# Performance work log

Measured on AMD Instinct MI355X. Metric: run time of the kernel, lower is better.

The kernel has to match this reference:

```python
import jax, jax.numpy as jnp
import numpy as np


def _mlp(x, w1, b1, w2, b2):
    # generic 2-layer MLP (stand-in for ConfiguredModule's combine_mlp / embedding_mlp)
    return jax.nn.gelu(x @ w1 + b1) @ w2 + b2


def setup_inputs() -> dict:
    key = jax.random.key(0)
    ks = jax.random.split(key, 8)
    B, N, A = 8, 128, 64          # molecules, atoms, nfeature
    Rr, Ra = 32, 16               # radial / angular geometry shifts
    P = N * (N - 1) // 2          # 8128 atom pairs
    d_pair, H, nembed = 32, 512, 256

    def rnd(k, shp, scale=1.0):
        return jax.random.normal(k, shp, dtype=jnp.float32) * scale

    return {
        "gr": rnd(ks[0], (B, N, Rr, N), 0.1),
        "ga": rnd(ks[1], (B, N, Ra, P), 0.1),
        "afv": rnd(ks[2], (B, N, A)),
        # combine_mlp: 2A -> 2A -> d_pair
        "cw1": rnd(ks[3], (2 * A, 2 * A), 1.0 / np.sqrt(2 * A)),
        "cb1": jnp.zeros((2 * A,), jnp.float32),
        "cw2": rnd(ks[4], (2 * A, d_pair), 1.0 / np.sqrt(2 * A)),
        "cb2": jnp.zeros((d_pair,), jnp.float32),
        # embedding_mlp: Rr*A + Ra*d_pair -> H -> nembed
        "ew1": rnd(ks[5], (Rr * A + Ra * d_pair, H), 1.0 / np.sqrt(Rr * A + Ra * d_pair)),
        "eb1": jnp.zeros((H,), jnp.float32),
        "ew2": rnd(ks[6], (H, nembed), 1.0 / np.sqrt(H)),
        "eb2": jnp.zeros((nembed,), jnp.float32),
    }


def reference(gr, ga, afv, cw1, cb1, cw2, cb2, ew1, eb1, ew2, eb2):
    B, N, A = afv.shape
    # _combine_afv_1: pairwise outer sum/product, upper-triangular (i<j) pairs.
    # Instead of materializing [B, 2A, N, N] and masking, gather pairs directly
    # (row-major i<j order matches torch's triu boolean-mask indexing).
    ii, jj = jnp.triu_indices(N, k=1)           # [P]
    ai = afv[:, ii, :]                           # [B, P, A]
    aj = afv[:, jj, :]                           # [B, P, A]
    afv_pair = jnp.concatenate([ai + aj, ai * aj], axis=-1)  # [B, P, 2A]
    afv_pair = _mlp(afv_pair, cw1, cb1, cw2, cb2)            # [B, P, d_pair]

    # grv = matmul(gr, afv[:, None]) : [B, N, Rr, N] @ [B, 1, N, A] -> [B, N, Rr, A]
    grv = jnp.einsum('bnrm,bma->bnra', gr, afv).reshape(B, N, -1)
    # gav = matmul(ga, afv_pair[:, None]) : [B, N, Ra, P] @ [B, 1, P, d] -> [B, N, Ra, d]
    gav = jnp.einsum('bnap,bpd->bnad', ga, afv_pair).reshape(B, N, -1)

    aef = _mlp(jnp.concatenate([grv, gav], axis=-1), ew1, eb1, ew2, eb2)  # [B, N, nembed]
    return aef, afv
```

## Files before the change

### kernel.cpp

```cpp
#include <hip/hip_runtime.h>
#include <math.h>

#define BB 8
#define NN 128
#define AA 64
#define RR 32
#define RA 16
#define PP 8128
#define DP 32
#define HH 512
#define EE 256
#define XDIM 2560

static constexpr size_t WS_PAIRT = 0;
static constexpr size_t WS_XB    = WS_PAIRT + (size_t)BB*DP*PP/2;
static constexpr size_t WS_EW1B  = WS_XB + (size_t)BB*NN*XDIM/2;
static constexpr size_t WS_AFVT  = WS_EW1B + (size_t)HH*XDIM/2;
static constexpr size_t WS_CW1T  = WS_AFVT + (size_t)BB*AA*NN/2;
static constexpr size_t WS_CW2T  = WS_CW1T + (size_t)128*128/2;
static constexpr size_t WS_EW2B  = WS_CW2T + (size_t)DP*128/2;
static constexpr size_t WS_HB    = WS_EW2B + (size_t)EE*HH/2;

typedef __attribute__((ext_vector_type(8))) short bf16x8;
typedef __attribute__((ext_vector_type(4))) float f32x4;

__device__ __forceinline__ float gelu_f(float x) {
    float u = 0.7978845608028654f * (x + 0.044715f * x * x * x);
    float au = fabsf(u);
    float e = __expf(-2.0f * au);
    float th = (1.0f - e) / (1.0f + e);
    th = copysignf(th, u);
    return 0.5f * x * (1.0f + th);
}

__device__ __forceinline__ unsigned short f2bf(float x) {
    union { float f; unsigned u; } v; v.f = x;
    unsigned r = v.u + 0x7fffu + ((v.u >> 16) & 1u);
    return (unsigned short)(r >> 16);
}

__device__ __forceinline__ bf16x8 pack_bf16x8(float4 a, float4 b) {
    bf16x8 r;
    r[0] = (short)f2bf(a.x); r[1] = (short)f2bf(a.y);
    r[2] = (short)f2bf(a.z); r[3] = (short)f2bf(a.w);
    r[4] = (short)f2bf(b.x); r[5] = (short)f2bf(b.y);
    r[6] = (short)f2bf(b.z); r[7] = (short)f2bf(b.w);
    return r;
}

__global__ __launch_bounds__(256) void prep_k(
    const float* __restrict__ afv, const float* __restrict__ cw1,
    const float* __restrict__ cw2, unsigned short* __restrict__ afvT,
    unsigned short* __restrict__ cw1T, unsigned short* __restrict__ cw2T,
    float* __restrict__ out2)
{
    const int bid = blockIdx.x, t = threadIdx.x;
    if (bid < 64) {
        int idx = bid * 256 + t;
        int b = idx >> 11;
        int rem = idx & 2047;
        int a = rem >> 5;
        int m0 = (rem & 31) * 4;
        ushort4 o;
        o.x = f2bf(afv[((size_t)b * NN + m0 + 0) * AA + a]);
        o.y = f2bf(afv[((size_t)b * NN + m0 + 1) * AA + a]);
        o.z = f2bf(afv[((size_t)b * NN + m0 + 2) * AA + a]);
        o.w = f2bf(afv[((size_t)b * NN + m0 + 3) * AA + a]);
        *(ushort4*)(afvT + ((size_t)b * AA + a) * NN + m0) = o;
        float4 v = *(const float4*)(afv + (size_t)idx * 4);
        *(float4*)(out2 + (size_t)idx * 4) = v;
    } else if (bid < 80) {
        int idx = (bid - 64) * 256 + t;
        int n = idx >> 5;
        int k0 = (idx & 31) * 4;
        ushort4 o;
        o.x = f2bf(cw1[(size_t)(k0 + 0) * 128 + n]);
        o.y = f2bf(cw1[(size_t)(k0 + 1) * 128 + n]);
        o.z = f2bf(cw1[(size_t)(k0 + 2) * 128 + n]);
        o.w = f2bf(cw1[(size_t)(k0 + 3) * 128 + n]);
        *(ushort4*)(cw1T + (size_t)n * 128 + k0) = o;
    } else {
        int idx = (bid - 80) * 256 + t;
        int d = idx >> 5;
        int k0 = (idx & 31) * 4;
        ushort4 o;
        o.x = f2bf(cw2[(size_t)(k0 + 0) * DP + d]);
        o.y = f2bf(cw2[(size_t)(k0 + 1) * DP + d]);
        o.z = f2bf(cw2[(size_t)(k0 + 2) * DP + d]);
        o.w = f2bf(cw2[(size_t)(k0 + 3) * DP + d]);
        *(ushort4*)(cw2T + (size_t)d * 128 + k0) = o;
    }
}

#define NB_GRV 256
#define NB_PAIR 1016

__global__ __launch_bounds__(256) void stage1_k(
    const float* __restrict__ afv, const unsigned short* __restrict__ cw1T,
    const float* __restrict__ cb1, const unsigned short* __restrict__ cw2T,
    const float* __restrict__ cb2, unsigned short* __restrict__ pairT,
    const float* __restrict__ gr, unsigned short* __restrict__ Xb,
    const unsigned short* __restrict__ afvT)
{
    __shared__ unsigned short sm[16384];
    __shared__ int iis[64], jjs[64];
    const int bid = blockIdx.x;
    const int t = threadIdx.x;
    const int w = t >> 6, lane = t & 63;
    const int lm = lane & 15, lg = lane >> 4;

    if (bid < NB_GRV) {
        const int b = bid >> 5;
        const int rbase = (bid & 31) * 128;
        const float* gab = gr + ((size_t)b * 4096 + rbase) * NN;
        unsigned short* As = sm;
        const int srow = t >> 1, half = t & 1;
        const float* arow = gab + (size_t)srow * NN + half * 64;
        #pragma unroll
        for (int q = 0; q < 8; ++q) {
            float4 x0 = *(const float4*)(arow + q * 8);
            float4 x1 = *(const float4*)(arow + q * 8 + 4);
            bf16x8 v = pack_bf16x8(x0, x1);
            int g = half * 8 + q;
            *(bf16x8*)(As + srow * 128 + ((g ^ (srow & 7)) * 8)) = v;
        }
        __syncthreads();
        const int wm = w * 32;
        f32x4 acc[2][4];
        #pragma unroll
        for (int i = 0; i < 2; ++i)
            #pragma unroll
            for (int j = 0; j < 4; ++j) acc[i][j] = 0.f;
        const unsigned short* Bb = afvT + (size_t)b * AA * NN;
        #pragma unroll
        for (int ks = 0; ks < 4; ++ks) {
            int g = ks * 4 + lg;
            int r0 = wm + lm, r1 = wm + 16 + lm;
            bf16x8 a0 = *(const bf16x8*)(As + r0 * 128 + ((g ^ (r0 & 7)) * 8));
            bf16x8 a1 = *(const bf16x8*)(As + r1 * 128 + ((g ^ (r1 & 7)) * 8));
            #pragma unroll
            for (int ni = 0; ni < 4; ++ni) {
                bf16x8 bv = *(const bf16x8*)(Bb + (size_t)(ni * 16 + lm) * NN + ks * 32 + lg * 8);
                acc[0][ni] = __builtin_amdgcn_mfma_f32_16x16x32_bf16(a0, bv, acc[0][ni], 0, 0, 0);
                acc[1][ni] = __builtin_amdgcn_mfma_f32_16x16x32_bf16(a1, bv, acc[1][ni], 0, 0, 0);
            }
        }
        __syncthreads();
        unsigned short* T = sm;
        #pragma unroll
        for (int mi = 0; mi < 2; ++mi)
            #pragma unroll
            for (int ni = 0; ni < 4; ++ni)
                #pragma unroll
                for (int r = 0; r < 4; ++r)
                    T[(wm + mi * 16 + lg * 4 + r) * 64 + ni * 16 + lm] =
                        f2bf(acc[mi][ni][r]);
        __syncthreads();
        #pragma unroll
        for (int q = 0; q < 4; ++q) {
            int idx = t + q * 256;
            int rr2 = idx >> 3, slot = idx & 7;
            bf16x8 v = *(const bf16x8*)(T + rr2 * 64 + slot * 8);
            int grow = rbase + rr2;
            *(bf16x8*)(Xb + ((size_t)(b * NN) + (grow >> 5)) * XDIM +
                       (grow & 31) * 64 + slot * 8) = v;
        }
        return;
    }

    const int bid2 = bid - NB_GRV;
    const int b = bid2 / 127;
    const int pbase = (bid2 % 127) * 64;
    unsigned short* X = sm;
    unsigned short* Hs = sm + 8192;

    if (t < 64) {
        int p = pbase + t;
        int i = 0;
        while (i < 126) {
            int nx = i + 1;
            int off = nx * 127 - (nx * (nx - 1)) / 2;
            if (off <= p) i = nx; else break;
        }
        int off = i * 127 - (i * (i - 1)) / 2;
        iis[t] = i;
        jjs[t] = i + 1 + (p - off);
    }
    __syncthreads();
    {
        int pp = t & 63, seg = t >> 6;
        const float* ar = afv + (size_t)(b * NN + iis[pp]) * AA + seg * 16;
        const float* br = afv + (size_t)(b * NN + jjs[pp]) * AA + seg * 16;
        float4 xa = *(const float4*)(ar),     xb2 = *(const float4*)(ar + 4);
        float4 xc = *(const float4*)(ar + 8), xd = *(const float4*)(ar + 12);
        float4 ya = *(const float4*)(br),     yb = *(const float4*)(br + 4);
        float4 yc = *(const float4*)(br + 8), yd = *(const float4*)(br + 12);
        float4 s0 = make_float4(xa.x + ya.x, xa.y + ya.y, xa.z + ya.z, xa.w + ya.w);
        float4 s1 = make_float4(xb2.x + yb.x, xb2.y + yb.y, xb2.z + yb.z, xb2.w + yb.w);
        float4 s2 = make_float4(xc.x + yc.x, xc.y + yc.y, xc.z + yc.z, xc.w + yc.w);
        float4 s3 = make_float4(xd.x + yd.x, xd.y + yd.y, xd.z + yd.z, xd.w + yd.w);
        float4 p0 = make_float4(xa.x * ya.x, xa.y * ya.y, xa.z * ya.z, xa.w * ya.w);
        float4 p1 = make_float4(xb2.x * yb.x, xb2.y * yb.y, xb2.z * yb.z, xb2.w * yb.w);
        float4 p2 = make_float4(xc.x * yc.x, xc.y * yc.y, xc.z * yc.z, xc.w * yc.w);
        float4 p3 = make_float4(xd.x * yd.x, xd.y * yd.y, xd.z * yd.z, xd.w * yd.w);
        int gs = seg * 2, gp = 8 + seg * 2, sw = pp & 7;
        *(bf16x8*)(X + pp * 128 + (((gs + 0) ^ sw) * 8)) = pack_bf16x8(s0, s1);
        *(bf16x8*)(X + pp * 128 + (((gs + 1) ^ sw) * 8)) = pack_bf16x8(s2, s3);
        *(bf16x8*)(X + pp * 128 + (((gp + 0) ^ sw) * 8)) = pack_bf16x8(p0, p1);
        *(bf16x8*)(X + pp * 128 + (((gp + 1) ^ sw) * 8)) = pack_bf16x8(p2, p3);
    }
    __syncthreads();
    const int wn = w * 32;
    f32x4 acc1[4][2];
    #pragma unroll
    for (int i = 0; i < 4; ++i)
        #pragma unroll
        for (int j = 0; j < 2; ++j) acc1[i][j] = 0.f;
    #pragma unroll
    for (int ks = 0; ks < 4; ++ks) {
        int g = ks * 4 + lg;
        bf16x8 a[4];
        #pragma unroll
        for (int mi = 0; mi < 4; ++mi) {
            int row = mi * 16 + lm;
            a[mi] = *(const bf16x8*)(X + row * 128 + ((g ^ (row & 7)) * 8));
        }
        #pragma unroll
        for (int ni = 0; ni < 2; ++ni) {
            bf16x8 bv = *(const bf16x8*)(cw1T + (size_t)(wn + ni * 16 + lm) * 128 +
                                         ks * 32 + lg * 8);
            #pragma unroll
            for (int mi = 0; mi < 4; ++mi)
                acc1[mi][ni] = __builtin_amdgcn_mfma_f32_16x16x32_bf16(
                    a[mi], bv, acc1[mi][ni], 0, 0, 0);
        }
    }
    #pragma unroll
    for (int ni = 0; ni < 2; ++ni) {
        int n = wn + ni * 16 + lm;
        float bb = cb1[n];
        int gn = n >> 3, ne = n & 7;
        #pragma unroll
        for (int mi = 0; mi < 4; ++mi)
            #pragma unroll
            for (int r = 0; r < 4; ++r) {
                int row = mi * 16 + lg * 4 + r;
                Hs[row * 128 + ((gn ^ (row & 7)) * 8 + ne)] =
                    f2bf(gelu_f(acc1[mi][ni][r] + bb));
            }
    }
    __syncthreads();
    f32x4 acc2[2];
    acc2[0] = 0.f; acc2[1] = 0.f;
    #pragma unroll
    for (int ks = 0; ks < 4; ++ks) {
        int row = w * 16 + lm;
        int g = ks * 4 + lg;
        bf16x8 a2 = *(const bf16x8*)(Hs + row * 128 + ((g ^ (row & 7)) * 8));
        #pragma unroll
        for (int ni = 0; ni < 2; ++ni) {
            bf16x8 bv = *(const bf16x8*)(cw2T + (size_t)(ni * 16 + lm) * 128 +
                                         ks * 32 + lg * 8);
            acc2[ni] = __builtin_amdgcn_mfma_f32_16x16x32_bf16(a2, bv, acc2[ni], 0, 0, 0);
        }
    }
    {
        unsigned short* T = sm;
        #pragma unroll
        for (int ni = 0; ni < 2; ++ni) {
            int d = ni * 16 + lm;
            float bb = cb2[d];
            #pragma unroll
            for (int r = 0; r < 4; ++r) {
                int p = w * 16 + lg * 4 + r;
                T[d * 64 + p] = f2bf(acc2[ni][r] + bb);
            }
        }
        __syncthreads();
        int d = t >> 3, slot = t & 7;
        bf16x8 v = *(const bf16x8*)(T + d * 64 + slot * 8);
        *(bf16x8*)(pairT + ((size_t)b * DP + d) * PP + pbase + slot * 8) = v;
    }
}

__global__ __launch_bounds__(256) void gav_k(
    const float* __restrict__ ga, const unsigned short* __restrict__ pairT,
    unsigned short* __restrict__ Xb,
    const float* __restrict__ ew1, unsigned short* __restrict__ ew1bT,
    const float* __restrict__ ew2, unsigned short* __restrict__ ew2bT)
{
    __shared__ unsigned short As[32 * 128];
    __shared__ unsigned short Bs[32 * 128];
    const int bid = blockIdx.x;
    const int t = threadIdx.x;

    if (bid >= 512 + 1280) {
        int q = (bid - (512 + 1280)) * 256 + t;
        int n = q & 255;
        int k0 = (q >> 8) * 4;
        ushort4 o;
        o.x = f2bf(ew2[(size_t)(k0 + 0) * EE + n]);
        o.y = f2bf(ew2[(size_t)(k0 + 1) * EE + n]);
        o.z = f2bf(ew2[(size_t)(k0 + 2) * EE + n]);
        o.w = f2bf(ew2[(size_t)(k0 + 3) * EE + n]);
        *(ushort4*)(ew2bT + (size_t)n * HH + k0) = o;
        return;
    }
    if (bid >= 512) {
        int q = (bid - 512) * 256 + t;
        int n = q & 511;
        int k0 = (q >> 9) * 4;
        ushort4 o;
        o.x = f2bf(ew1[(size_t)(k0 + 0) * HH + n]);
        o.y = f2bf(ew1[(size_t)(k0 + 1) * HH + n]);
        o.z = f2bf(ew1[(size_t)(k0 + 2) * HH + n]);
        o.w = f2bf(ew1[(size_t)(k0 + 3) * HH + n]);
        *(ushort4*)(ew1bT + (size_t)n * XDIM + k0) = o;
        return;
    }

    const int rt = bid & 63, b = bid >> 6;
    const int rbase = rt * 32;
    const int srow = t >> 3, slot = t & 7;
    const int w = t >> 6, lane = t & 63;
    const int lm = lane & 15, lg = lane >> 4;
    const int wr = (w & 1) * 16, wc = (w >> 1) * 16;

    f32x4 acc = 0.f;

    const float* gab = ga + (size_t)(b * 2048 + rbase) * PP;
    const unsigned short* pbT = pairT + (size_t)b * DP * PP;

    float4 ra[4];
    bf16x8 rb0, rb1;
    {
        int k0 = slot * 8;
        ra[0] = *(const float4*)(gab + (size_t)srow * PP + k0);
        ra[1] = *(const float4*)(gab + (size_t)srow * PP + k0 + 4);
        ra[2] = *(const float4*)(gab + (size_t)srow * PP + k0 + 64);
        ra[3] = *(const float4*)(gab + (size_t)srow * PP + k0 + 68);
        rb0 = *(const bf16x8*)(pbT + (size_t)srow * PP + k0);
        rb1 = *(const bf16x8*)(pbT + (size_t)srow * PP + k0 + 64);
    }

    for (int it = 0; it < 64; ++it) {
        __syncthreads();
        const int sw = srow & 7;
        const int g0 = (slot ^ sw) * 8;
        const int g1 = ((slot ^ sw) + 8) * 8;
        *(bf16x8*)(As + srow * 128 + g0) = pack_bf16x8(ra[0], ra[1]);
        *(bf16x8*)(As + srow * 128 + g1) = pack_bf16x8(ra[2], ra[3]);
        *(bf16x8*)(Bs + srow * 128 + g0) = rb0;
        *(bf16x8*)(Bs + srow * 128 + g1) = rb1;
        __syncthreads();
        if (it + 1 < 64) {
            int kn = (it + 1) * 128 + slot * 8;
            int k1 = kn + 64; if (k1 > PP - 8) k1 = PP - 8;
            ra[0] = *(const float4*)(gab + (size_t)srow * PP + kn);
            ra[1] = *(const float4*)(gab + (size_t)srow * PP + kn + 4);
            ra[2] = *(const float4*)(gab + (size_t)srow * PP + k1);
            ra[3] = *(const float4*)(gab + (size_t)srow * PP + k1 + 4);
            rb0 = *(const bf16x8*)(pbT + (size_t)srow * PP + kn);
            rb1 = *(const bf16x8*)(pbT + (size_t)srow * PP + k1);
        }
        if (it < 63) {
            #pragma unroll
            for (int ks = 0; ks < 4; ++ks) {
                int gg = ks * 4 + lg;
                int rowa = wr + lm;
                int rowb = wc + lm;
                bf16x8 a  = *(const bf16x8*)(As + rowa * 128 + ((gg ^ (rowa & 7)) * 8));
                bf16x8 bv = *(const bf16x8*)(Bs + rowb * 128 + ((gg ^ (rowb & 7)) * 8));
                acc = __builtin_amdgcn_mfma_f32_16x16x32_bf16(a, bv, acc, 0, 0, 0);
            }
        } else {
            #pragma unroll
            for (int ks = 0; ks < 2; ++ks) {
                int gg = ks * 4 + lg;
                int rowa = wr + lm;
                int rowb = wc + lm;
                bf16x8 a  = *(const bf16x8*)(As + rowa * 128 + ((gg ^ (rowa & 7)) * 8));
                bf16x8 bv = *(const bf16x8*)(Bs + rowb * 128 + ((gg ^ (rowb & 7)) * 8));
                acc = __builtin_amdgcn_mfma_f32_16x16x32_bf16(a, bv, acc, 0, 0, 0);
            }
        }
    }
    #pragma unroll
    for (int r = 0; r < 4; ++r) {
        int grow = rbase + wr + lg * 4 + r;
        int n = grow >> 4, a2 = grow & 15;
        int d = wc + lm;
        Xb[(size_t)(b * NN + n) * XDIM + 2048 + a2 * DP + d] = f2bf(acc[r]);
    }
}

__global__ __launch_bounds__(256) void mlp1_k(
    const unsigned short* __restrict__ Xb,
    const unsigned short* __restrict__ Wt,
    const float* __restrict__ eb1, unsigned short* __restrict__ Hb)
{
    __shared__ unsigned short As[32 * 64];
    __shared__ unsigned short Bs[64 * 64];
    const int bid = blockIdx.x;
    const int ct = bid & 7, rt = bid >> 3;
    const int rbase = rt * 32, nbase = ct * 64;
    const int t = threadIdx.x;
    const int w = t >> 6, lane = t & 63;
    const int lm = lane & 15, lg = lane >> 4;
    const int srow = t >> 3, sg = t & 7;

    f32x4 acc[2];
    acc[0] = 0.f; acc[1] = 0.f;

    const unsigned short* Arow  = Xb + (size_t)(rbase + srow) * XDIM;
    const unsigned short* Brow0 = Wt + (size_t)(nbase + srow) * XDIM;
    const unsigned short* Brow1 = Wt + (size_t)(nbase + srow + 32) * XDIM;

    bf16x8 rA, rB0, rB1;
    rA  = *(const bf16x8*)(Arow + sg * 8);
    rB0 = *(const bf16x8*)(Brow0 + sg * 8);
    rB1 = *(const bf16x8*)(Brow1 + sg * 8);

    for (int it = 0; it < 40; ++it) {
        __syncthreads();
        const int sw = srow & 7;
        *(bf16x8*)(As + srow * 64 + ((sg ^ sw) * 8)) = rA;
        *(bf16x8*)(Bs + srow * 64 + ((sg ^ sw) * 8)) = rB0;
        *(bf16x8*)(Bs + (srow + 32) * 64 + ((sg ^ sw) * 8)) = rB1;
        __syncthreads();
        if (it + 1 < 40) {
            int kn = (it + 1) * 64;
            rA  = *(const bf16x8*)(Arow + kn + sg * 8);
            rB0 = *(const bf16x8*)(Brow0 + kn + sg * 8);
            rB1 = *(const bf16x8*)(Brow1 + kn + sg * 8);
        }
        #pragma unroll
        for (int ks = 0; ks < 2; ++ks) {
            int g = ks * 4 + lg;
            int r0 = lm, r1 = 16 + lm, rb_ = w * 16 + lm;
            bf16x8 a0 = *(const bf16x8*)(As + r0 * 64 + ((g ^ (r0 & 7)) * 8));
            bf16x8 a1 = *(const bf16x8*)(As + r1 * 64 + ((g ^ (r1 & 7)) * 8));
            bf16x8 bv = *(const bf16x8*)(Bs + rb_ * 64 + ((g ^ (rb_ & 7)) * 8));
            acc[0] = __builtin_amdgcn_mfma_f32_16x16x32_bf16(a0, bv, acc[0], 0, 0, 0);
            acc[1] = __builtin_amdgcn_mfma_f32_16x16x32_bf16(a1, bv, acc[1], 0, 0, 0);
        }
    }
    const int col = nbase + w * 16 + lm;
    const float bb = eb1[col];
    #pragma unroll
    for (int mi = 0; mi < 2; ++mi)
        #pragma unroll
        for (int r = 0; r < 4; ++r) {
            int row = rbase + mi * 16 + lg * 4 + r;
            Hb[(size_t)row * HH + col] = f2bf(gelu_f(acc[mi][r] + bb));
        }
}

__global__ __launch_bounds__(256) void mlp2_k(
    const unsigned short* __restrict__ Hb,
    const unsigned short* __restrict__ Wt,
    const float* __restrict__ eb2, float* __restrict__ out)
{
    __shared__ unsigned short As[32 * 64];
    __shared__ unsigned short Bs[64 * 64];
    const int bid = blockIdx.x;
    const int ct = bid & 3, rt = bid >> 2;
    const int rbase = rt * 32, nbase = ct * 64;
    const int t = threadIdx.x;
    const int w = t >> 6, lane = t & 63;
    const int lm = lane & 15, lg = lane >> 4;
    const int srow = t >> 3, sg = t & 7;

    f32x4 acc[2];
    acc[0] = 0.f; acc[1] = 0.f;

    const unsigned short* Arow  = Hb + (size_t)(rbase + srow) * HH;
    const unsigned short* Brow0 = Wt + (size_t)(nbase + srow) * HH;
    const unsigned short* Brow1 = Wt + (size_t)(nbase + srow + 32) * HH;

    bf16x8 rA, rB0, rB1;
    rA  = *(const bf16x8*)(Arow + sg * 8);
    rB0 = *(const bf16x8*)(Brow0 + sg * 8);
    rB1 = *(const bf16x8*)(Brow1 + sg * 8);

    for (int it = 0; it < 8; ++it) {
        __syncthreads();
        const int sw = srow & 7;
        *(bf16x8*)(As + srow * 64 + ((sg ^ sw) * 8)) = rA;
        *(bf16x8*)(Bs + srow * 64 + ((sg ^ sw) * 8)) = rB0;
        *(bf16x8*)(Bs + (srow + 32) * 64 + ((sg ^ sw) * 8)) = rB1;
        __syncthreads();
        if (it + 1 < 8) {
            int kn = (it + 1) * 64;
            rA  = *(const bf16x8*)(Arow + kn + sg * 8);
            rB0 = *(const bf16x8*)(Brow0 + kn + sg * 8);
            rB1 = *(const bf16x8*)(Brow1 + kn + sg * 8);
        }
        #pragma unroll
        for (int ks = 0; ks < 2; ++ks) {
            int g = ks * 4 + lg;
            int r0 = lm, r1 = 16 + lm, rb_ = w * 16 + lm;
            bf16x8 a0 = *(const bf16x8*)(As + r0 * 64 + ((g ^ (r0 & 7)) * 8));
            bf16x8 a1 = *(const bf16x8*)(As + r1 * 64 + ((g ^ (r1 & 7)) * 8));
            bf16x8 bv = *(const bf16x8*)(Bs + rb_ * 64 + ((g ^ (rb_ & 7)) * 8));
            acc[0] = __builtin_amdgcn_mfma_f32_16x16x32_bf16(a0, bv, acc[0], 0, 0, 0);
            acc[1] = __builtin_amdgcn_mfma_f32_16x16x32_bf16(a1, bv, acc[1], 0, 0, 0);
        }
    }
    const int col = nbase + w * 16 + lm;
    const float bb = eb2[col];
    #pragma unroll
    for (int mi = 0; mi < 2; ++mi)
        #pragma unroll
        for (int r = 0; r < 4; ++r) {
            int row = rbase + mi * 16 + lg * 4 + r;
            out[(size_t)row * EE + col] = acc[mi][r] + bb;
        }
}

extern "C" void kernel_launch(void* const* d_in, const int* in_sizes, int n_in,
                              void* d_out, int out_size, void* d_ws, size_t ws_size,
                              hipStream_t stream) {
    const float* gr  = (const float*)d_in[0];
    const float* ga  = (const float*)d_in[1];
    const float* afv = (const float*)d_in[2];
    const float* cw1 = (const float*)d_in[3];
    const float* cb1 = (const float*)d_in[4];
    const float* cw2 = (const float*)d_in[5];
    const float* cb2 = (const float*)d_in[6];
    const float* ew1 = (const float*)d_in[7];
    const float* eb1 = (const float*)d_in[8];
    const float* ew2 = (const float*)d_in[9];
    const float* eb2 = (const float*)d_in[10];
    float* out = (float*)d_out;
    float* ws = (float*)d_ws;

    unsigned short* pairT  = (unsigned short*)(ws + WS_PAIRT);
    unsigned short* Xb     = (unsigned short*)(ws + WS_XB);
    unsigned short* ew1bT  = (unsigned short*)(ws + WS_EW1B);
    unsigned short* afvT   = (unsigned short*)(ws + WS_AFVT);
    unsigned short* cw1T   = (unsigned short*)(ws + WS_CW1T);
    unsigned short* cw2T   = (unsigned short*)(ws + WS_CW2T);
    unsigned short* ew2bT  = (unsigned short*)(ws + WS_EW2B);
    unsigned short* Hb     = (unsigned short*)(ws + WS_HB);

    prep_k<<<dim3(84), dim3(256), 0, stream>>>(afv, cw1, cw2, afvT, cw1T, cw2T,
                                               out + (size_t)BB * NN * EE);
    stage1_k<<<dim3(NB_GRV + NB_PAIR), dim3(256), 0, stream>>>(
        afv, cw1T, cb1, cw2T, cb2, pairT, gr, Xb, afvT);
    gav_k<<<dim3(1920), dim3(256), 0, stream>>>(ga, pairT, Xb, ew1, ew1bT, ew2, ew2bT);
    mlp1_k<<<dim3(256), dim3(256), 0, stream>>>(Xb, ew1bT, eb1, Hb);
    mlp2_k<<<dim3(128), dim3(256), 0, stream>>>(Hb, ew2bT, eb2, out);
}
```

Measured before the change: 187.7 us.

## Move grv GEMM into gav kernel and shrink MLP tiles for more blocks

The gr×afv GEMM moves out of stage1 into the gav kernel. afv is now transposed to bf16 in shared memory inside each block, so the separate afvT prep pass and its workspace go away. The afv passthrough copy also moves into gav_k. The gav blocks are reindexed so batch is the fastest-varying index. The MLP1 and MLP2 kernels use 32x32 output tiles instead of 32x64, doubling the grid size for better CU occupancy at the cost of reloading the A operand more often.

```diff
diff --git a/kernel.cpp b/kernel.cpp
--- a/kernel.cpp
+++ b/kernel.cpp
@@ -15,8 +15,7 @@
 static constexpr size_t WS_PAIRT = 0;
 static constexpr size_t WS_XB    = WS_PAIRT + (size_t)BB*DP*PP/2;
 static constexpr size_t WS_EW1B  = WS_XB + (size_t)BB*NN*XDIM/2;
-static constexpr size_t WS_AFVT  = WS_EW1B + (size_t)HH*XDIM/2;
-static constexpr size_t WS_CW1T  = WS_AFVT + (size_t)BB*AA*NN/2;
+static constexpr size_t WS_CW1T  = WS_EW1B + (size_t)HH*XDIM/2;
 static constexpr size_t WS_CW2T  = WS_CW1T + (size_t)128*128/2;
 static constexpr size_t WS_EW2B  = WS_CW2T + (size_t)DP*128/2;
 static constexpr size_t WS_HB    = WS_EW2B + (size_t)EE*HH/2;
@@ -49,28 +48,12 @@
 }
 
 __global__ __launch_bounds__(256) void prep_k(
-    const float* __restrict__ afv, const float* __restrict__ cw1,
-    const float* __restrict__ cw2, unsigned short* __restrict__ afvT,
-    unsigned short* __restrict__ cw1T, unsigned short* __restrict__ cw2T,
-    float* __restrict__ out2)
+    const float* __restrict__ cw1, const float* __restrict__ cw2,
+    unsigned short* __restrict__ cw1T, unsigned short* __restrict__ cw2T)
 {
     const int bid = blockIdx.x, t = threadIdx.x;
-    if (bid < 64) {
+    if (bid < 16) {
         int idx = bid * 256 + t;
-        int b = idx >> 11;
-        int rem = idx & 2047;
-        int a = rem >> 5;
-        int m0 = (rem & 31) * 4;
-        ushort4 o;
-        o.x = f2bf(afv[((size_t)b * NN + m0 + 0) * AA + a]);
-        o.y = f2bf(afv[((size_t)b * NN + m0 + 1) * AA + a]);
-        o.z = f2bf(afv[((size_t)b * NN + m0 + 2) * AA + a]);
-        o.w = f2bf(afv[((size_t)b * NN + m0 + 3) * AA + a]);
-        *(ushort4*)(afvT + ((size_t)b * AA + a) * NN + m0) = o;
-        float4 v = *(const float4*)(afv + (size_t)idx * 4);
-        *(float4*)(out2 + (size_t)idx * 4) = v;
-    } else if (bid < 80) {
-        int idx = (bid - 64) * 256 + t;
         int n = idx >> 5;
         int k0 = (idx & 31) * 4;
         ushort4 o;
@@ -80,7 +63,7 @@
         o.w = f2bf(cw1[(size_t)(k0 + 3) * 128 + n]);
         *(ushort4*)(cw1T + (size_t)n * 128 + k0) = o;
     } else {
-        int idx = (bid - 80) * 256 + t;
+        int idx = (bid - 16) * 256 + t;
         int d = idx >> 5;
         int k0 = (idx & 31) * 4;
         ushort4 o;
@@ -92,15 +75,10 @@
     }
 }
 
-#define NB_GRV 256
-#define NB_PAIR 1016
-
 __global__ __launch_bounds__(256) void stage1_k(
     const float* __restrict__ afv, const unsigned short* __restrict__ cw1T,
     const float* __restrict__ cb1, const unsigned short* __restrict__ cw2T,
-    const float* __restrict__ cb2, unsigned short* __restrict__ pairT,
-    const float* __restrict__ gr, unsigned short* __restrict__ Xb,
-    const unsigned short* __restrict__ afvT)
+    const float* __restrict__ cb2, unsigned short* __restrict__ pairT)
 {
     __shared__ unsigned short sm[16384];
     __shared__ int iis[64], jjs[64];
@@ -109,68 +87,8 @@
     const int w = t >> 6, lane = t & 63;
     const int lm = lane & 15, lg = lane >> 4;
 
-    if (bid < NB_GRV) {
-        const int b = bid >> 5;
-        const int rbase = (bid & 31) * 128;
-        const float* gab = gr + ((size_t)b * 4096 + rbase) * NN;
-        unsigned short* As = sm;
-        const int srow = t >> 1, half = t & 1;
-        const float* arow = gab + (size_t)srow * NN + half * 64;
-        #pragma unroll
-        for (int q = 0; q < 8; ++q) {
-            float4 x0 = *(const float4*)(arow + q * 8);
-            float4 x1 = *(const float4*)(arow + q * 8 + 4);
-            bf16x8 v = pack_bf16x8(x0, x1);
-            int g = half * 8 + q;
-            *(bf16x8*)(As + srow * 128 + ((g ^ (srow & 7)) * 8)) = v;
-        }
-        __syncthreads();
-        const int wm = w * 32;
-        f32x4 acc[2][4];
-        #pragma unroll
-        for (int i = 0; i < 2; ++i)
-            #pragma unroll
-            for (int j = 0; j < 4; ++j) acc[i][j] = 0.f;
-        const unsigned short* Bb = afvT + (size_t)b * AA * NN;
-        #pragma unroll
-        for (int ks = 0; ks < 4; ++ks) {
-            int g = ks * 4 + lg;
-            int r0 = wm + lm, r1 = wm + 16 + lm;
-            bf16x8 a0 = *(const bf16x8*)(As + r0 * 128 + ((g ^ (r0 & 7)) * 8));
-            bf16x8 a1 = *(const bf16x8*)(As + r1 * 128 + ((g ^ (r1 & 7)) * 8));
-            #pragma unroll
-            for (int ni = 0; ni < 4; ++ni) {
-                bf16x8 bv = *(const bf16x8*)(Bb + (size_t)(ni * 16 + lm) * NN + ks * 32 + lg * 8);
-                acc[0][ni] = __builtin_amdgcn_mfma_f32_16x16x32_bf16(a0, bv, acc[0][ni], 0, 0, 0);
-                acc[1][ni] = __builtin_amdgcn_mfma_f32_16x16x32_bf16(a1, bv, acc[1][ni], 0, 0, 0);
-            }
-        }
-        __syncthreads();
-        unsigned short* T = sm;
-        #pragma unroll
-        for (int mi = 0; mi < 2; ++mi)
-            #pragma unroll
-            for (int ni = 0; ni < 4; ++ni)
-                #pragma unroll
-                for (int r = 0; r < 4; ++r)
-                    T[(wm + mi * 16 + lg * 4 + r) * 64 + ni * 16 + lm] =
-                        f2bf(acc[mi][ni][r]);
-        __syncthreads();
-        #pragma unroll
-        for (int q = 0; q < 4; ++q) {
-            int idx = t + q * 256;
-            int rr2 = idx >> 3, slot = idx & 7;
-            bf16x8 v = *(const bf16x8*)(T + rr2 * 64 + slot * 8);
-            int grow = rbase + rr2;
-            *(bf16x8*)(Xb + ((size_t)(b * NN) + (grow >> 5)) * XDIM +
-                       (grow & 31) * 64 + slot * 8) = v;
-        }
-        return;
-    }
-
-    const int bid2 = bid - NB_GRV;
-    const int b = bid2 / 127;
-    const int pbase = (bid2 % 127) * 64;
+    const int b = bid / 127;
+    const int pbase = (bid % 127) * 64;
     unsigned short* X = sm;
     unsigned short* Hs = sm + 8192;
 
@@ -266,6 +184,7 @@
     }
     {
         unsigned short* T = sm;
+        __syncthreads();
         #pragma unroll
         for (int ni = 0; ni < 2; ++ni) {
             int d = ni * 16 + lm;
@@ -286,16 +205,25 @@
 __global__ __launch_bounds__(256) void gav_k(
     const float* __restrict__ ga, const unsigned short* __restrict__ pairT,
     unsigned short* __restrict__ Xb,
+    const float* __restrict__ gr, const float* __restrict__ afv,
     const float* __restrict__ ew1, unsigned short* __restrict__ ew1bT,
-    const float* __restrict__ ew2, unsigned short* __restrict__ ew2bT)
+    const float* __restrict__ ew2, unsigned short* __restrict__ ew2bT,
+    float* __restrict__ out2)
 {
-    __shared__ unsigned short As[32 * 128];
-    __shared__ unsigned short Bs[32 * 128];
+    __shared__ unsigned short sm[24576];
     const int bid = blockIdx.x;
     const int t = threadIdx.x;
-
-    if (bid >= 512 + 1280) {
-        int q = (bid - (512 + 1280)) * 256 + t;
+    const int w = t >> 6, lane = t & 63;
+    const int lm = lane & 15, lg = lane >> 4;
+
+    if (bid >= 2176) {
+        int idx = (bid - 2176) * 256 + t;
+        float4 v = *(const float4*)(afv + (size_t)idx * 4);
+        *(float4*)(out2 + (size_t)idx * 4) = v;
+        return;
+    }
+    if (bid >= 2048) {
+        int q = (bid - 2048) * 256 + t;
         int n = q & 255;
         int k0 = (q >> 8) * 4;
         ushort4 o;
@@ -306,8 +234,8 @@
         *(ushort4*)(ew2bT + (size_t)n * HH + k0) = o;
         return;
     }
-    if (bid >= 512) {
-        int q = (bid - 512) * 256 + t;
+    if (bid >= 768) {
+        int q = (bid - 768) * 256 + t;
         int n = q & 511;
         int k0 = (q >> 9) * 4;
         ushort4 o;
@@ -319,12 +247,88 @@
         return;
     }
 
-    const int rt = bid & 63, b = bid >> 6;
+    if (bid >= 512) {
+        const int gb = bid - 512;
+        const int b = gb >> 5;
+        const int rbase = (gb & 31) * 128;
+        const float* gab = gr + ((size_t)b * 4096 + rbase) * NN;
+        unsigned short* As  = sm;
+        unsigned short* Bs2 = sm + 16384;
+        {
+            const int srow = t >> 1, half = t & 1;
+            const float* arow = gab + (size_t)srow * NN + half * 64;
+            #pragma unroll
+            for (int q = 0; q < 8; ++q) {
+                float4 x0 = *(const float4*)(arow + q * 8);
+                float4 x1 = *(const float4*)(arow + q * 8 + 4);
+                bf16x8 v = pack_bf16x8(x0, x1);
+                int g = half * 8 + q;
+                *(bf16x8*)(As + srow * 128 + ((g ^ (srow & 7)) * 8)) = v;
+            }
+        }
+        #pragma unroll
+        for (int q = 0; q < 8; ++q) {
+            int pos = t + q * 256;
+            int m = pos >> 4, f4i = pos & 15;
+            float4 v = *(const float4*)(afv + (size_t)(b * NN + m) * AA + f4i * 4);
+            int gm = m >> 3, me = m & 7;
+            float vv[4] = {v.x, v.y, v.z, v.w};
+            #pragma unroll
+            for (int i = 0; i < 4; ++i) {
+                int a = f4i * 4 + i;
+                Bs2[a * 128 + ((gm ^ (a & 7)) * 8 + me)] = f2bf(vv[i]);
+            }
+        }
+        __syncthreads();
+        const int wm = w * 32;
+        f32x4 acc[2][4];
+        #pragma unroll
+        for (int i = 0; i < 2; ++i)
+            #pragma unroll
+            for (int j = 0; j < 4; ++j) acc[i][j] = 0.f;
+        #pragma unroll
+        for (int ks = 0; ks < 4; ++ks) {
+            int g = ks * 4 + lg;
+            int r0 = wm + lm, r1 = wm + 16 + lm;
+            bf16x8 a0 = *(const bf16x8*)(As + r0 * 128 + ((g ^ (r0 & 7)) * 8));
+            bf16x8 a1 = *(const bf16x8*)(As + r1 * 128 + ((g ^ (r1 & 7)) * 8));
+            #pragma unroll
+            for (int ni = 0; ni < 4; ++ni) {
+                int a = ni * 16 + lm;
+                bf16x8 bv = *(const bf16x8*)(Bs2 + a * 128 + ((g ^ (a & 7)) * 8));
+                acc[0][ni] = __builtin_amdgcn_mfma_f32_16x16x32_bf16(a0, bv, acc[0][ni], 0, 0, 0);
+                acc[1][ni] = __builtin_amdgcn_mfma_f32_16x16x32_bf16(a1, bv, acc[1][ni], 0, 0, 0);
+            }
+        }
+        __syncthreads();
+        unsigned short* T = sm;
+        #pragma unroll
+        for (int mi = 0; mi < 2; ++mi)
+            #pragma unroll
+            for (int ni = 0; ni < 4; ++ni)
+                #pragma unroll
+                for (int r = 0; r < 4; ++r)
+                    T[(wm + mi * 16 + lg * 4 + r) * 64 + ni * 16 + lm] =
+                        f2bf(acc[mi][ni][r]);
+        __syncthreads();
+        #pragma unroll
+        for (int q = 0; q < 4; ++q) {
+            int idx = t + q * 256;
+            int rr2 = idx >> 3, slot = idx & 7;
+            bf16x8 v = *(const bf16x8*)(T + rr2 * 64 + slot * 8);
+            int grow = rbase + rr2;
+            *(bf16x8*)(Xb + ((size_t)(b * NN) + (grow >> 5)) * XDIM +
+                       (grow & 31) * 64 + slot * 8) = v;
+        }
+        return;
+    }
+
+    const int b = bid & 7, rt = bid >> 3;
     const int rbase = rt * 32;
     const int srow = t >> 3, slot = t & 7;
-    const int w = t >> 6, lane = t & 63;
-    const int lm = lane & 15, lg = lane >> 4;
     const int wr = (w & 1) * 16, wc = (w >> 1) * 16;
+    unsigned short* As = sm;
+    unsigned short* Bs = sm + 4096;
 
     f32x4 acc = 0.f;
 
@@ -400,60 +404,51 @@
     const float* __restrict__ eb1, unsigned short* __restrict__ Hb)
 {
     __shared__ unsigned short As[32 * 64];
-    __shared__ unsigned short Bs[64 * 64];
+    __shared__ unsigned short Bs[32 * 64];
     const int bid = blockIdx.x;
-    const int ct = bid & 7, rt = bid >> 3;
-    const int rbase = rt * 32, nbase = ct * 64;
+    const int ct = bid & 15, rt = bid >> 4;
+    const int rbase = rt * 32, nbase = ct * 32;
     const int t = threadIdx.x;
     const int w = t >> 6, lane = t & 63;
     const int lm = lane & 15, lg = lane >> 4;
+    const int wr = (w & 1) * 16, wc = (w >> 1) * 16;
     const int srow = t >> 3, sg = t & 7;
 
-    f32x4 acc[2];
-    acc[0] = 0.f; acc[1] = 0.f;
-
-    const unsigned short* Arow  = Xb + (size_t)(rbase + srow) * XDIM;
-    const unsigned short* Brow0 = Wt + (size_t)(nbase + srow) * XDIM;
-    const unsigned short* Brow1 = Wt + (size_t)(nbase + srow + 32) * XDIM;
-
-    bf16x8 rA, rB0, rB1;
-    rA  = *(const bf16x8*)(Arow + sg * 8);
-    rB0 = *(const bf16x8*)(Brow0 + sg * 8);
-    rB1 = *(const bf16x8*)(Brow1 + sg * 8);
+    f32x4 acc = 0.f;
+
+    const unsigned short* Arow = Xb + (size_t)(rbase + srow) * XDIM;
+    const unsigned short* Brow = Wt + (size_t)(nbase + srow) * XDIM;
+
+    bf16x8 rA = *(const bf16x8*)(Arow + sg * 8);
+    bf16x8 rB = *(const bf16x8*)(Brow + sg * 8);
 
     for (int it = 0; it < 40; ++it) {
         __syncthreads();
         const int sw = srow & 7;
         *(bf16x8*)(As + srow * 64 + ((sg ^ sw) * 8)) = rA;
-        *(bf16x8*)(Bs + srow * 64 + ((sg ^ sw) * 8)) = rB0;
-        *(bf16x8*)(Bs + (srow + 32) * 64 + ((sg ^ sw) * 8)) = rB1;
+        *(bf16x8*)(Bs + srow * 64 + ((sg ^ sw) * 8)) = rB;
         __syncthreads();
         if (it + 1 < 40) {
             int kn = (it + 1) * 64;
-            rA  = *(const bf16x8*)(Arow + kn + sg * 8);
-            rB0 = *(const bf16x8*)(Brow0 + kn + sg * 8);
-            rB1 = *(const bf16x8*)(Brow1 + kn + sg * 8);
+            rA = *(const bf16x8*)(Arow + kn + sg * 8);
+            rB = *(const bf16x8*)(Brow + kn + sg * 8);
         }
         #pragma unroll
         for (int ks = 0; ks < 2; ++ks) {
             int g = ks * 4 + lg;
-            int r0 = lm, r1 = 16 + lm, rb_ = w * 16 + lm;
-            bf16x8 a0 = *(const bf16x8*)(As + r0 * 64 + ((g ^ (r0 & 7)) * 8));
-            bf16x8 a1 = *(const bf16x8*)(As + r1 * 64 + ((g ^ (r1 & 7)) * 8));
-            bf16x8 bv = *(const bf16x8*)(Bs + rb_ * 64 + ((g ^ (rb_ & 7)) * 8));
-            acc[0] = __builtin_amdgcn_mfma_f32_16x16x32_bf16(a0, bv, acc[0], 0, 0, 0);
-            acc[1] = __builtin_amdgcn_mfma_f32_16x16x32_bf16(a1, bv, acc[1], 0, 0, 0);
-        }
-    }
-    const int col = nbase + w * 16 + lm;
+            int r0 = wr + lm, r1 = wc + lm;
+            bf16x8 a  = *(const bf16x8*)(As + r0 * 64 + ((g ^ (r0 & 7)) * 8));
+            bf16x8 bv = *(const bf16x8*)(Bs + r1 * 64 + ((g ^ (r1 & 7)) * 8));
+            acc = __builtin_amdgcn_mfma_f32_16x16x32_bf16(a, bv, acc, 0, 0, 0);
+        }
+    }
+    const int col = nbase + wc + lm;
     const float bb = eb1[col];
     #pragma unroll
-    for (int mi = 0; mi < 2; ++mi)
-        #pragma unroll
-        for (int r = 0; r < 4; ++r) {
-            int row = rbase + mi * 16 + lg * 4 + r;
-            Hb[(size_t)row * HH + col] = f2bf(gelu_f(acc[mi][r] + bb));
-        }
+    for (int r = 0; r < 4; ++r) {
+        int row = rbase + wr + lg * 4 + r;
+        Hb[(size_t)row * HH + col] = f2bf(gelu_f(acc[r] + bb));
+    }
 }
 
 __global__ __launch_bounds__(256) void mlp2_k(
@@ -462,60 +457,51 @@
     const float* __restrict__ eb2, float* __restrict__ out)
 {
     __shared__ unsigned short As[32 * 64];
-    __shared__ unsigned short Bs[64 * 64];
+    __shared__ unsigned short Bs[32 * 64];
     const int bid = blockIdx.x;
-    const int ct = bid & 3, rt = bid >> 2;
-    const int rbase = rt * 32, nbase = ct * 64;
+    const int ct = bid & 7, rt = bid >> 3;
+    const int rbase = rt * 32, nbase = ct * 32;
     const int t = threadIdx.x;
     const int w = t >> 6, lane = t & 63;
     const int lm = lane & 15, lg = lane >> 4;
+    const int wr = (w & 1) * 16, wc = (w >> 1) * 16;
     const int srow = t >> 3, sg = t & 7;
 
-    f32x4 acc[2];
-    acc[0] = 0.f; acc[1] = 0.f;
-
-    const unsigned short* Arow  = Hb + (size_t)(rbase + srow) * HH;
-    const unsigned short* Brow0 = Wt + (size_t)(nbase + srow) * HH;
-    const unsigned short* Brow1 = Wt + (size_t)(nbase + srow + 32) * HH;
-
-    bf16x8 rA, rB0, rB1;
-    rA  = *(const bf16x8*)(Arow + sg * 8);
-    rB0 = *(const bf16x8*)(Brow0 + sg * 8);
-    rB1 = *(const bf16x8*)(Brow1 + sg * 8);
+    f32x4 acc = 0.f;
+
+    const unsigned short* Arow = Hb + (size_t)(rbase + srow) * HH;
+    const unsigned short* Brow = Wt + (size_t)(nbase + srow) * HH;
+
+    bf16x8 rA = *(const bf16x8*)(Arow + sg * 8);
+    bf16x8 rB = *(const bf16x8*)(Brow + sg * 8);
 
     for (int it = 0; it < 8; ++it) {
         __syncthreads();
         const int sw = srow & 7;
         *(bf16x8*)(As + srow * 64 + ((sg ^ sw) * 8)) = rA;
-        *(bf16x8*)(Bs + srow * 64 + ((sg ^ sw) * 8)) = rB0;
-        *(bf16x8*)(Bs + (srow + 32) * 64 + ((sg ^ sw) * 8)) = rB1;
+        *(bf16x8*)(Bs + srow * 64 + ((sg ^ sw) * 8)) = rB;
         __syncthreads();
         if (it + 1 < 8) {
             int kn = (it + 1) * 64;
-            rA  = *(const bf16x8*)(Arow + kn + sg * 8);
-            rB0 = *(const bf16x8*)(Brow0 + kn + sg * 8);
-            rB1 = *(const bf16x8*)(Brow1 + kn + sg * 8);
+            rA = *(const bf16x8*)(Arow + kn + sg * 8);
+            rB = *(const bf16x8*)(Brow + kn + sg * 8);
         }
         #pragma unroll
         for (int ks = 0; ks < 2; ++ks) {
             int g = ks * 4 + lg;
-            int r0 = lm, r1 = 16 + lm, rb_ = w * 16 + lm;
-            bf16x8 a0 = *(const bf16x8*)(As + r0 * 64 + ((g ^ (r0 & 7)) * 8));
-            bf16x8 a1 = *(const bf16x8*)(As + r1 * 64 + ((g ^ (r1 & 7)) * 8));
-            bf16x8 bv = *(const bf16x8*)(Bs + rb_ * 64 + ((g ^ (rb_ & 7)) * 8));
-            acc[0] = __builtin_amdgcn_mfma_f32_16x16x32_bf16(a0, bv, acc[0], 0, 0, 0);
-            acc[1] = __builtin_amdgcn_mfma_f32_16x16x32_bf16(a1, bv, acc[1], 0, 0, 0);
-        }
-    }
-    const int col = nbase + w * 16 + lm;
+            int r0 = wr + lm, r1 = wc + lm;
+            bf16x8 a  = *(const bf16x8*)(As + r0 * 64 + ((g ^ (r0 & 7)) * 8));
+            bf16x8 bv = *(const bf16x8*)(Bs + r1 * 64 + ((g ^ (r1 & 7)) * 8));
+            acc = __builtin_amdgcn_mfma_f32_16x16x32_bf16(a, bv, acc, 0, 0, 0);
+        }
+    }
+    const int col = nbase + wc + lm;
     const float bb = eb2[col];
     #pragma unroll
-    for (int mi = 0; mi < 2; ++mi)
-        #pragma unroll
-        for (int r = 0; r < 4; ++r) {
-            int row = rbase + mi * 16 + lg * 4 + r;
-            out[(size_t)row * EE + col] = acc[mi][r] + bb;
-        }
+    for (int r = 0; r < 4; ++r) {
+        int row = rbase + wr + lg * 4 + r;
+        out[(size_t)row * EE + col] = acc[r] + bb;
+    }
 }
 
 extern "C" void kernel_launch(void* const* d_in, const int* in_sizes, int n_in,
@@ -538,17 +524,16 @@
     unsigned short* pairT  = (unsigned short*)(ws + WS_PAIRT);
     unsigned short* Xb     = (unsigned short*)(ws + WS_XB);
     unsigned short* ew1bT  = (unsigned short*)(ws + WS_EW1B);
-    unsigned short* afvT   = (unsigned short*)(ws + WS_AFVT);
     unsigned short* cw1T   = (unsigned short*)(ws + WS_CW1T);
     unsigned short* cw2T   = (unsigned short*)(ws + WS_CW2T);
     unsigned short* ew2bT  = (unsigned short*)(ws + WS_EW2B);
     unsigned short* Hb     = (unsigned short*)(ws + WS_HB);
 
-    prep_k<<<dim3(84), dim3(256), 0, stream>>>(afv, cw1, cw2, afvT, cw1T, cw2T,
-                                               out + (size_t)BB * NN * EE);
-    stage1_k<<<dim3(NB_GRV + NB_PAIR), dim3(256), 0, stream>>>(
-        afv, cw1T, cb1, cw2T, cb2, pairT, gr, Xb, afvT);
-    gav_k<<<dim3(1920), dim3(256), 0, stream>>>(ga, pairT, Xb, ew1, ew1bT, ew2, ew2bT);
-    mlp1_k<<<dim3(256), dim3(256), 0, stream>>>(Xb, ew1bT, eb1, Hb);
-    mlp2_k<<<dim3(128), dim3(256), 0, stream>>>(Hb, ew2bT, eb2, out);
-}
+    prep_k<<<dim3(20), dim3(256), 0, stream>>>(cw1, cw2, cw1T, cw2T);
+    stage1_k<<<dim3(1016), dim3(256), 0, stream>>>(afv, cw1T, cb1, cw2T, cb2, pairT);
+    gav_k<<<dim3(2240), dim3(256), 0, stream>>>(ga, pairT, Xb, gr, afv,
+                                                ew1, ew1bT, ew2, ew2bT,
+                                                out + (size_t)BB * NN * EE);
+    mlp1_k<<<dim3(512), dim3(256), 0, stream>>>(Xb, ew1bT, eb1, Hb);
+    mlp2_k<<<dim3(256), dim3(256), 0, stream>>>(Hb, ew2bT, eb2, out);
+}
```

Result: faster. 180.7 us (-3.7%).
